# Performance work log

Hardware: AMD Instinct MI355X
Metric: run time of the kernel (lower is better)

Reference implementation:

```python
import jax, jax.numpy as jnp
import numpy as np

B, G, H = 16, 1708, 5


def setup_inputs() -> dict:
    key = jax.random.key(0)
    k0, k1, k2, k3 = jax.random.split(key, 4)
    x = jax.random.normal(k0, (B, G), dtype=jnp.float32)
    # xavier_normal on (H, G, 1): std = gain*sqrt(2/(fan_in+fan_out)) ~ gain*sqrt(2/G)
    std_qk = 5.0 * np.sqrt(2.0 / (G + 1))   # gain=5 for WQ, WK
    std_v = 1.0 * np.sqrt(2.0 / (G + 1))    # gain=1 for WV
    WQ = jax.random.normal(k1, (H, G, 1), dtype=jnp.float32) * std_qk
    WK = jax.random.normal(k2, (H, G, 1), dtype=jnp.float32) * std_qk
    WV = jax.random.normal(k3, (H, G, 1), dtype=jnp.float32) * std_v
    W0 = jnp.ones((H,), dtype=jnp.float32)  # torch.Tensor(n_head*[1])
    return {"x": x, "WQ": WQ, "WK": WK, "WV": WV, "W0": W0}


def reference(x, WQ, WK, WV, W0):
    # x: (B, G); WQ/WK/WV: (H, G, 1); W0: (H,)
    g = x.shape[1]
    off_diag = 1.0 - jnp.eye(g, dtype=x.dtype)  # mask applied AFTER softmax
    head_outs = []
    for h in range(WQ.shape[0]):  # small fixed head loop keeps peak memory low
        q = x * WQ[h, :, 0]  # (B, G)
        k = x * WK[h, :, 0]  # (B, G)
        v = x * WV[h, :, 0]  # (B, G)
        # scores[b,i,j] = q[b,i] * k[b,j]  (broadcast outer product, not dot-product)
        scores = q[:, :, None] * k[:, None, :]  # (B, G, G)
        z = jax.nn.softmax(scores, axis=2) * off_diag
        head_outs.append(jnp.einsum('bij,bj->bi', z, v))  # (B, G)
    out_seq = jnp.stack(head_outs, axis=-1)  # (B, G, H)
    return jnp.einsum('bgh,h->bg', out_seq, W0)  # (B, G)
```

## Files before the change

kernel.cpp:

```cpp
#include <hip/hip_runtime.h>

constexpr int B = 16;
constexpr int G = 1708;
constexpr int H = 5;
constexpr int M1 = 17;
constexpr int JS = 4;
constexpr int JPS = G / JS;
constexpr int TPB1 = 256;
constexpr int TPB2 = 64;

#define LOG2E 1.4426950408889634f


__device__ __forceinline__ float fast_exp(float x) {
#if __has_builtin(__builtin_amdgcn_exp2f)
    return __builtin_amdgcn_exp2f(x * LOG2E);
#else
    return __expf(x);
#endif
}

__constant__ float INVFACT[M1] = {
    (float)(1.0),                    (float)(1.0),
    (float)(1.0 / 2.0),              (float)(1.0 / 6.0),
    (float)(1.0 / 24.0),             (float)(1.0 / 120.0),
    (float)(1.0 / 720.0),            (float)(1.0 / 5040.0),
    (float)(1.0 / 40320.0),          (float)(1.0 / 362880.0),
    (float)(1.0 / 3628800.0),        (float)(1.0 / 39916800.0),
    (float)(1.0 / 479001600.0),      (float)(1.0 / 6227020800.0),
    (float)(1.0 / 87178291200.0),    (float)(1.0 / 1307674368000.0),
    (float)(1.0 / 20922789888000.0)
};

__global__ __launch_bounds__(TPB1)
void moments_kernel(const float* __restrict__ x,
                    const float* __restrict__ WK,
                    const float* __restrict__ WV,
                    float* __restrict__ g_mom)
{
    const int slice = blockIdx.x % JS;
    const int h     = (blockIdx.x / JS) % H;
    const int b     = blockIdx.x / (JS * H);
    const int j0    = slice * JPS;

    const float* __restrict__ xb = x  + b * G;
    const float* __restrict__ wk = WK + h * G;
    const float* __restrict__ wv = WV + h * G;

    float S[M1], T[M1];
#pragma unroll
    for (int m = 0; m < M1; ++m) { S[m] = 0.f; T[m] = 0.f; }

    for (int t = threadIdx.x; t < JPS; t += TPB1) {
        const int j   = j0 + t;
        const float xj = xb[j];
        const float k  = xj * wk[j];
        const float v  = xj * wv[j];
        const float k2 = k * k;
        const float k4 = k2 * k2;
        float p0 = 1.f, p1 = k, p2 = k2, p3 = k2 * k;
#pragma unroll
        for (int gblk = 0; gblk < 4; ++gblk) {
            const int base = gblk * 4;
            S[base + 0] += p0; T[base + 0] = fmaf(v, p0, T[base + 0]); p0 *= k4;
            S[base + 1] += p1; T[base + 1] = fmaf(v, p1, T[base + 1]); p1 *= k4;
            S[base + 2] += p2; T[base + 2] = fmaf(v, p2, T[base + 2]); p2 *= k4;
            S[base + 3] += p3; T[base + 3] = fmaf(v, p3, T[base + 3]); p3 *= k4;
        }
        S[16] += p0; T[16] = fmaf(v, p0, T[16]);
    }

#pragma unroll
    for (int m = 0; m < M1; ++m) {
#pragma unroll
        for (int off = 8; off <= 32; off <<= 1) {
            S[m] += __shfl_xor(S[m], off, 64);
            T[m] += __shfl_xor(T[m], off, 64);
        }
    }

    __shared__ float red[4 * 8][2 * M1];
    const int wave = threadIdx.x >> 6;
    const int lane = threadIdx.x & 63;
    if (lane < 8) {
        const int row = wave * 8 + lane;
#pragma unroll
        for (int m = 0; m < M1; ++m) {
            red[row][m]      = S[m];
            red[row][M1 + m] = T[m];
        }
    }
    __syncthreads();

    if (threadIdx.x < 2 * M1) {
        const int m = threadIdx.x % M1;
        float s0 = 0.f, s1 = 0.f, s2 = 0.f, s3 = 0.f;
#pragma unroll
        for (int r = 0; r < 32; r += 4) {
            s0 += red[r + 0][threadIdx.x];
            s1 += red[r + 1][threadIdx.x];
            s2 += red[r + 2][threadIdx.x];
            s3 += red[r + 3][threadIdx.x];
        }
        const float s = ((s0 + s1) + (s2 + s3)) * INVFACT[m];
        atomicAdd(&g_mom[(b * H + h) * (2 * M1) + threadIdx.x], s);
    }
}

__global__ __launch_bounds__(TPB2)
void eval_kernel(const float* __restrict__ x,
                 const float* __restrict__ WQ,
                 const float* __restrict__ WK,
                 const float* __restrict__ WV,
                 const float* __restrict__ W0,
                 const float* __restrict__ g_mom,
                 float* __restrict__ out)
{
    const int b = blockIdx.y;
    const int i = blockIdx.x * TPB2 + threadIdx.x;
    if (i >= G) return;

    const float xi = x[b * G + i];
    float acc = 0.f;

#pragma unroll
    for (int h = 0; h < H; ++h) {
        const float* __restrict__ mp = g_mom + (b * H + h) * (2 * M1);
        const float q = xi * WQ[h * G + i];

        float D = mp[M1 - 1];
        float N = mp[2 * M1 - 1];
#pragma unroll
        for (int m = M1 - 2; m >= 0; --m) {
            D = fmaf(D, q, mp[m]);
            N = fmaf(N, q, mp[M1 + m]);
        }

        const float k   = xi * WK[h * G + i];
        const float v   = xi * WV[h * G + i];
        const float eii = fast_exp(q * k);
        acc = fmaf(W0[h], (N - eii * v) / D, acc);
    }
    out[b * G + i] = acc;
}

extern "C" void kernel_launch(void* const* d_in, const int* in_sizes, int n_in,
                              void* d_out, int out_size, void* d_ws, size_t ws_size,
                              hipStream_t stream) {
    const float* x  = (const float*)d_in[0];
    const float* WQ = (const float*)d_in[1];
    const float* WK = (const float*)d_in[2];
    const float* WV = (const float*)d_in[3];
    const float* W0 = (const float*)d_in[4];
    float* out   = (float*)d_out;
    float* g_mom = (float*)d_ws;

    hipMemsetAsync(g_mom, 0, (size_t)(B * H * 2 * M1) * sizeof(float), stream);

    moments_kernel<<<B * H * JS, TPB1, 0, stream>>>(x, WK, WV, g_mom);

    dim3 grid2((G + TPB2 - 1) / TPB2, B);
    eval_kernel<<<grid2, TPB2, 0, stream>>>(x, WQ, WK, WV, W0, g_mom, out);
}
```

Measured before the change: 69.60 us.

## Fuse moment accumulation and evaluation into a single kernel per batch tile

Replaces the memset, the atomic moment-reduction kernel and the evaluation kernel with one fused kernel. Each block covering a (tile, batch) pair recomputes the full Taylor moments for all heads in shared memory and then evaluates its slice of outputs. This removes two launches, the memset and the global atomics. In exchange every tile block redundantly recomputes the moments over all of G, and the grid shrinks to 64 blocks of 512 threads, giving lower parallelism on a large GPU.

```diff
diff --git a/kernel.cpp b/kernel.cpp
--- a/kernel.cpp
+++ b/kernel.cpp
@@ -1,13 +1,13 @@
 #include <hip/hip_runtime.h>
 
-constexpr int B = 16;
-constexpr int G = 1708;
-constexpr int H = 5;
+constexpr int B  = 16;
+constexpr int G  = 1708;
+constexpr int H  = 5;
 constexpr int M1 = 17;
-constexpr int JS = 4;
-constexpr int JPS = G / JS;
-constexpr int TPB1 = 256;
-constexpr int TPB2 = 64;
+constexpr int TPB = 512;
+constexpr int NW  = TPB / 64;
+constexpr int RR  = NW * 8;
+constexpr int TILES = (G + TPB - 1) / TPB;
 
 #define LOG2E 1.4426950408889634f
 
@@ -32,116 +32,113 @@
     (float)(1.0 / 20922789888000.0)
 };
 
-__global__ __launch_bounds__(TPB1)
-void moments_kernel(const float* __restrict__ x,
-                    const float* __restrict__ WK,
-                    const float* __restrict__ WV,
-                    float* __restrict__ g_mom)
+__global__ __launch_bounds__(TPB)
+void fused_kernel(const float* __restrict__ x,
+                  const float* __restrict__ WQ,
+                  const float* __restrict__ WK,
+                  const float* __restrict__ WV,
+                  const float* __restrict__ W0,
+                  float* __restrict__ out)
 {
-    const int slice = blockIdx.x % JS;
-    const int h     = (blockIdx.x / JS) % H;
-    const int b     = blockIdx.x / (JS * H);
-    const int j0    = slice * JPS;
+    __shared__ float xs[G];
+    __shared__ float red[H][RR][2 * M1];
+    __shared__ float mom[H][2 * M1];
 
-    const float* __restrict__ xb = x  + b * G;
-    const float* __restrict__ wk = WK + h * G;
-    const float* __restrict__ wv = WV + h * G;
+    const int tile = blockIdx.x;
+    const int b    = blockIdx.y;
+    const int tid  = threadIdx.x;
+    const int lane = tid & 63;
+    const int wave = tid >> 6;
 
-    float S[M1], T[M1];
+    const float* __restrict__ xb = x + b * G;
+    for (int t = tid; t < G; t += TPB) xs[t] = xb[t];
+    __syncthreads();
+
+#pragma unroll 1
+    for (int h = 0; h < H; ++h) {
+        const float* __restrict__ wk = WK + h * G;
+        const float* __restrict__ wv = WV + h * G;
+
+        float S[M1], T[M1];
 #pragma unroll
-    for (int m = 0; m < M1; ++m) { S[m] = 0.f; T[m] = 0.f; }
+        for (int m = 0; m < M1; ++m) { S[m] = 0.f; T[m] = 0.f; }
 
-    for (int t = threadIdx.x; t < JPS; t += TPB1) {
-        const int j   = j0 + t;
-        const float xj = xb[j];
-        const float k  = xj * wk[j];
-        const float v  = xj * wv[j];
-        const float k2 = k * k;
-        const float k4 = k2 * k2;
-        float p0 = 1.f, p1 = k, p2 = k2, p3 = k2 * k;
+        for (int t = tid; t < G; t += TPB) {
+            const float xj = xs[t];
+            const float k  = xj * wk[t];
+            const float v  = xj * wv[t];
+            const float k2 = k * k;
+            const float k4 = k2 * k2;
+            float p0 = 1.f, p1 = k, p2 = k2, p3 = k2 * k;
 #pragma unroll
-        for (int gblk = 0; gblk < 4; ++gblk) {
-            const int base = gblk * 4;
-            S[base + 0] += p0; T[base + 0] = fmaf(v, p0, T[base + 0]); p0 *= k4;
-            S[base + 1] += p1; T[base + 1] = fmaf(v, p1, T[base + 1]); p1 *= k4;
-            S[base + 2] += p2; T[base + 2] = fmaf(v, p2, T[base + 2]); p2 *= k4;
-            S[base + 3] += p3; T[base + 3] = fmaf(v, p3, T[base + 3]); p3 *= k4;
+            for (int gblk = 0; gblk < 4; ++gblk) {
+                const int base = gblk * 4;
+                S[base + 0] += p0; T[base + 0] = fmaf(v, p0, T[base + 0]); p0 *= k4;
+                S[base + 1] += p1; T[base + 1] = fmaf(v, p1, T[base + 1]); p1 *= k4;
+                S[base + 2] += p2; T[base + 2] = fmaf(v, p2, T[base + 2]); p2 *= k4;
+                S[base + 3] += p3; T[base + 3] = fmaf(v, p3, T[base + 3]); p3 *= k4;
+            }
+            S[16] += p0; T[16] = fmaf(v, p0, T[16]);
         }
-        S[16] += p0; T[16] = fmaf(v, p0, T[16]);
-    }
 
 #pragma unroll
-    for (int m = 0; m < M1; ++m) {
+        for (int m = 0; m < M1; ++m) {
 #pragma unroll
-        for (int off = 8; off <= 32; off <<= 1) {
-            S[m] += __shfl_xor(S[m], off, 64);
-            T[m] += __shfl_xor(T[m], off, 64);
+            for (int off = 8; off <= 32; off <<= 1) {
+                S[m] += __shfl_xor(S[m], off, 64);
+                T[m] += __shfl_xor(T[m], off, 64);
+            }
         }
-    }
-
-    __shared__ float red[4 * 8][2 * M1];
-    const int wave = threadIdx.x >> 6;
-    const int lane = threadIdx.x & 63;
-    if (lane < 8) {
-        const int row = wave * 8 + lane;
+        if (lane < 8) {
+            const int r = wave * 8 + lane;
 #pragma unroll
-        for (int m = 0; m < M1; ++m) {
-            red[row][m]      = S[m];
-            red[row][M1 + m] = T[m];
+            for (int m = 0; m < M1; ++m) {
+                red[h][r][m]      = S[m];
+                red[h][r][M1 + m] = T[m];
+            }
         }
     }
     __syncthreads();
 
-    if (threadIdx.x < 2 * M1) {
-        const int m = threadIdx.x % M1;
+    if (tid < H * 2 * M1) {
+        const int h = tid / (2 * M1);
+        const int c = tid % (2 * M1);
         float s0 = 0.f, s1 = 0.f, s2 = 0.f, s3 = 0.f;
 #pragma unroll
-        for (int r = 0; r < 32; r += 4) {
-            s0 += red[r + 0][threadIdx.x];
-            s1 += red[r + 1][threadIdx.x];
-            s2 += red[r + 2][threadIdx.x];
-            s3 += red[r + 3][threadIdx.x];
+        for (int r = 0; r < RR; r += 4) {
+            s0 += red[h][r + 0][c];
+            s1 += red[h][r + 1][c];
+            s2 += red[h][r + 2][c];
+            s3 += red[h][r + 3][c];
         }
-        const float s = ((s0 + s1) + (s2 + s3)) * INVFACT[m];
-        atomicAdd(&g_mom[(b * H + h) * (2 * M1) + threadIdx.x], s);
+        const int m = (c < M1) ? c : (c - M1);
+        mom[h][c] = ((s0 + s1) + (s2 + s3)) * INVFACT[m];
     }
-}
+    __syncthreads();
 
-__global__ __launch_bounds__(TPB2)
-void eval_kernel(const float* __restrict__ x,
-                 const float* __restrict__ WQ,
-                 const float* __restrict__ WK,
-                 const float* __restrict__ WV,
-                 const float* __restrict__ W0,
-                 const float* __restrict__ g_mom,
-                 float* __restrict__ out)
-{
-    const int b = blockIdx.y;
-    const int i = blockIdx.x * TPB2 + threadIdx.x;
-    if (i >= G) return;
+    const int i = tile * TPB + tid;
+    if (i < G) {
+        const float xi = xs[i];
+        float acc = 0.f;
+#pragma unroll
+        for (int h = 0; h < H; ++h) {
+            const float q = xi * WQ[h * G + i];
 
-    const float xi = x[b * G + i];
-    float acc = 0.f;
+            float D = mom[h][M1 - 1];
+            float N = mom[h][2 * M1 - 1];
+#pragma unroll
+            for (int m = M1 - 2; m >= 0; --m) {
+                D = fmaf(D, q, mom[h][m]);
+                N = fmaf(N, q, mom[h][M1 + m]);
+            }
 
-#pragma unroll
-    for (int h = 0; h < H; ++h) {
-        const float* __restrict__ mp = g_mom + (b * H + h) * (2 * M1);
-        const float q = xi * WQ[h * G + i];
-
-        float D = mp[M1 - 1];
-        float N = mp[2 * M1 - 1];
-#pragma unroll
-        for (int m = M1 - 2; m >= 0; --m) {
-            D = fmaf(D, q, mp[m]);
-            N = fmaf(N, q, mp[M1 + m]);
+            const float k   = xi * WK[h * G + i];
+            const float v   = xi * WV[h * G + i];
+            const float eii = fast_exp(q * k);
+            acc = fmaf(W0[h], (N - eii * v) / D, acc);
         }
-
-        const float k   = xi * WK[h * G + i];
-        const float v   = xi * WV[h * G + i];
-        const float eii = fast_exp(q * k);
-        acc = fmaf(W0[h], (N - eii * v) / D, acc);
+        out[b * G + i] = acc;
     }
-    out[b * G + i] = acc;
 }
 
 extern "C" void kernel_launch(void* const* d_in, const int* in_sizes, int n_in,
@@ -152,13 +149,8 @@
     const float* WK = (const float*)d_in[2];
     const float* WV = (const float*)d_in[3];
     const float* W0 = (const float*)d_in[4];
-    float* out   = (float*)d_out;
-    float* g_mom = (float*)d_ws;
+    float* out = (float*)d_out;
 
-    hipMemsetAsync(g_mom, 0, (size_t)(B * H * 2 * M1) * sizeof(float), stream);
-
-    moments_kernel<<<B * H * JS, TPB1, 0, stream>>>(x, WK, WV, g_mom);
-
-    dim3 grid2((G + TPB2 - 1) / TPB2, B);
-    eval_kernel<<<grid2, TPB2, 0, stream>>>(x, WQ, WK, WV, W0, g_mom, out);
+    dim3 grid(TILES, B);
+    fused_kernel<<<grid, TPB, 0, stream>>>(x, WQ, WK, WV, W0, out);
 }
```

New measurement: 78.10 us. 12.2% more time.
